# Kernel optimization log

Measured on AMD Instinct MI355X. Metric: run time of the kernel, lower is better.

Reference implementation:

```python
import jax, jax.numpy as jnp
import numpy as np

B, S, D, H, DFF, L, V, LAT = 2, 1800, 128, 8, 512, 6, 16, 1024
DK = D // H


def _pos_encoding():
    # PositionalEncoding buffer, deterministic
    pos = jnp.arange(S, dtype=jnp.float32)[:, None]
    div = jnp.exp(jnp.arange(0, D, 2, dtype=jnp.float32) * (-np.log(10000.0) / D))
    pe = jnp.zeros((S, D), jnp.float32)
    pe = pe.at[:, 0::2].set(jnp.sin(pos * div))
    pe = pe.at[:, 1::2].set(jnp.cos(pos * div))
    return pe  # [S, D]


def _layernorm(x, g, b, eps=1e-5):
    mu = jnp.mean(x, axis=-1, keepdims=True)
    var = jnp.mean((x - mu) ** 2, axis=-1, keepdims=True)
    return (x - mu) / jnp.sqrt(var + eps) * g + b


def _mha(xq, xkv, wq, bq, wk, bk, wv, bv, wo, bo, mask):
    Bq, Sq, _ = xq.shape
    Sk = xkv.shape[1]
    Q = (xq @ wq + bq).reshape(Bq, Sq, H, DK)
    K = (xkv @ wk + bk).reshape(Bq, Sk, H, DK)
    Vv = (xkv @ wv + bv).reshape(Bq, Sk, H, DK)
    scores = jnp.einsum('bqhd,bkhd->bhqk', Q, K) / np.sqrt(DK)
    if mask is not None:
        # faithful to source: masked_fill(mask==0, -1e9) keeps only j>i
        scores = jnp.where(mask, scores, -1e9)
    attn = jax.nn.softmax(scores, axis=-1)
    out = jnp.einsum('bhqk,bkhd->bqhd', attn, Vv).reshape(Bq, Sq, D)
    return out @ wo + bo


def setup_inputs():
    key = jax.random.key(0)
    ks = iter(jax.random.split(key, 40))

    def w(shape, fan_in):
        return (jax.random.normal(next(ks), shape, jnp.float32) / np.sqrt(fan_in))

    inp = {
        'latent': jax.random.normal(next(ks), (B, LAT), jnp.float32),
        'lp_w1': w((LAT, 2 * D), LAT), 'lp_b1': jnp.zeros((2 * D,), jnp.float32),
        'lp_w2': w((2 * D, D * S), 2 * D), 'lp_b2': jnp.zeros((D * S,), jnp.float32),
        'out_w': w((D, V), D), 'out_b': jnp.zeros((V,), jnp.float32),
    }
    for pfx in ('sa', 'ca'):
        for nm in ('q', 'k', 'v', 'o'):
            inp[f'{pfx}_w{nm}'] = w((L, D, D), D)
            inp[f'{pfx}_b{nm}'] = jnp.zeros((L, D), jnp.float32)
    inp['ff_w1'] = w((L, D, DFF), D)
    inp['ff_b1'] = jnp.zeros((L, DFF), jnp.float32)
    inp['ff_w2'] = w((L, DFF, D), DFF)
    inp['ff_b2'] = jnp.zeros((L, D), jnp.float32)
    for i in (1, 2, 3):
        inp[f'ln{i}_g'] = jnp.ones((L, D), jnp.float32)
        inp[f'ln{i}_b'] = jnp.zeros((L, D), jnp.float32)
    return inp


def reference(latent, lp_w1, lp_b1, lp_w2, lp_b2,
              sa_wq, sa_bq, sa_wk, sa_bk, sa_wv, sa_bv, sa_wo, sa_bo,
              ca_wq, ca_bq, ca_wk, ca_bk, ca_wv, ca_bv, ca_wo, ca_bo,
              ff_w1, ff_b1, ff_w2, ff_b2,
              ln1_g, ln1_b, ln2_g, ln2_b, ln3_g, ln3_b,
              out_w, out_b):
    # latent projection -> [B, S, D]
    h = jax.nn.relu(latent @ lp_w1 + lp_b1)
    dec = (h @ lp_w2 + lp_b2).reshape(B, S, D)
    dec = dec + _pos_encoding()[None, :, :]
    # source bug reproduced: only strictly-upper-triangle positions attend
    tgt_mask = jnp.triu(jnp.ones((S, S), bool), 1)
    enc = dec
    x = dec
    for i in range(L):
        a = _mha(x, x, sa_wq[i], sa_bq[i], sa_wk[i], sa_bk[i],
                 sa_wv[i], sa_bv[i], sa_wo[i], sa_bo[i], tgt_mask)
        x = _layernorm(x + a, ln1_g[i], ln1_b[i])
        c = _mha(x, enc, ca_wq[i], ca_bq[i], ca_wk[i], ca_bk[i],
                 ca_wv[i], ca_bv[i], ca_wo[i], ca_bo[i], None)
        x = _layernorm(x + c, ln2_g[i], ln2_b[i])
        f = jax.nn.relu(x @ ff_w1[i] + ff_b1[i]) @ ff_w2[i] + ff_b2[i]
        x = _layernorm(x + f, ln3_g[i], ln3_b[i])
    return x @ out_w + out_b  # [B, S, V]
```

## Files before the change

kernel.cpp:

```cpp
#include <hip/hip_runtime.h>
#include <hip/hip_bf16.h>
#include <math.h>

#define Bn   2
#define Sn   1800
#define Dn   128
#define Hn   8
#define DKn  16
#define DFFn 512
#define Ln   6
#define Vn   16
#define LATn 1024
#define BSn  3600
#define SDn  230400
#define NQT  57
#define VTJ  1824
#define MPAD 3712

typedef __attribute__((ext_vector_type(8))) short short8;
typedef __attribute__((ext_vector_type(16))) float f32x16;
typedef unsigned int u32;
typedef unsigned short u16;

#define ROWMAP(r, hi) (((r) & 3) + 8 * ((r) >> 2) + 4 * (hi))
#define GPERM(sl) (((sl) & 3) + (((sl) & 4) << 1) + (((sl) & 8) >> 1) + ((sl) & 16))

__device__ inline u32 cvtpk_bf16(float a, float b) {
    u32 r;
    asm("v_cvt_pk_bf16_f32 %0, %1, %2" : "=v"(r) : "v"(a), "v"(b));
    return r;
}

__device__ inline u16 f2bf(float f) {
    union { float f; u32 u; } x; x.f = f;
    u32 r = (x.u + 0x7FFFu + ((x.u >> 16) & 1u)) >> 16;
    return (u16)r;
}

__device__ inline float bf2f(u16 v) {
    union { u32 u; float f; } x; x.u = ((u32)v) << 16;
    return x.f;
}

__global__ __launch_bounds__(256) void wconv8_kernel(
    const float* __restrict__ s0, const float* __restrict__ s1,
    const float* __restrict__ s2, const float* __restrict__ s3,
    const float* __restrict__ s4, const float* __restrict__ s5,
    const float* __restrict__ s6, const float* __restrict__ s7,
    u16* __restrict__ d0, u16* __restrict__ d1, u16* __restrict__ d2,
    u16* __restrict__ d3, u16* __restrict__ d4, u16* __restrict__ d5,
    u16* __restrict__ d6, u16* __restrict__ d7)
{
    const int z = blockIdx.z;
    const float* src = (z == 0) ? s0 : (z == 1) ? s1 : (z == 2) ? s2 : (z == 3) ? s3
                     : (z == 4) ? s4 : (z == 5) ? s5 : (z == 6) ? s6 : s7;
    u16* dst = (z == 0) ? d0 : (z == 1) ? d1 : (z == 2) ? d2 : (z == 3) ? d3
             : (z == 4) ? d4 : (z == 5) ? d5 : (z == 6) ? d6 : d7;
    const int id = blockIdx.x * 256 + threadIdx.x;
    const int l = id >> 14, rem = id & 16383;
    const int n = rem >> 7, k = rem & 127;
    dst[id] = f2bf(src[l * 16384 + k * 128 + n]);
}

__global__ __launch_bounds__(256) void wconvg_kernel(
    const float* __restrict__ src, u16* __restrict__ dst, int logK, int logN)
{
    const int id = blockIdx.x * 256 + threadIdx.x;
    const int kn = 1 << (logK + logN);
    const int l = id >> (logK + logN);
    const int rem = id & (kn - 1);
    const int n = rem >> logK, k = rem & ((1 << logK) - 1);
    dst[id] = f2bf(src[(size_t)l * kn + (k << logN) + n]);
}

__global__ __launch_bounds__(256) void zvt_kernel(u16* __restrict__ Vt)
{
    const int id = blockIdx.x * 256 + threadIdx.x;
    const int row = id >> 5, pos = id & 31;
    Vt[(size_t)row * VTJ + 1792 + pos] = 0;
}

__global__ __launch_bounds__(256) void lat_h_kernel(
    const float* __restrict__ latent, const float* __restrict__ w1,
    const float* __restrict__ b1, float* __restrict__ h)
{
    __shared__ float ls[LATn];
    const int b = blockIdx.x;
    const int t = threadIdx.x;
    for (int k = t; k < LATn; k += 256) ls[k] = latent[b * LATn + k];
    __syncthreads();
    float acc = 0.f;
    #pragma unroll 8
    for (int k = 0; k < LATn; ++k) acc = fmaf(ls[k], w1[(size_t)k * 256 + t], acc);
    h[b * 256 + t] = fmaxf(acc + b1[t], 0.f);
}

__global__ __launch_bounds__(256) void dec_kernel(
    const float* __restrict__ h, const float* __restrict__ w2,
    const float* __restrict__ b2, float* __restrict__ x,
    u16* __restrict__ xb, u16* __restrict__ encb)
{
    __shared__ float hs[512];
    const int t = threadIdx.x;
    hs[t] = h[t];
    hs[256 + t] = h[256 + t];
    __syncthreads();
    const int j = blockIdx.x * 256 + t;
    float a0 = 0.f, a1 = 0.f;
    #pragma unroll 8
    for (int k = 0; k < 256; ++k) {
        float w = w2[(size_t)k * SDn + j];
        a0 = fmaf(hs[k], w, a0);
        a1 = fmaf(hs[256 + k], w, a1);
    }
    const int s = j >> 7, d = j & 127;
    const int i2 = d >> 1;
    const float freq = __expf(-(float)(2 * i2) * (9.210340371976184f / 128.f));
    const float ang = (float)s * freq;
    const float pe = (d & 1) ? cosf(ang) : sinf(ang);
    const float bias = b2[j] + pe;
    const float v0 = a0 + bias;
    const float v1 = a1 + bias;
    x[j] = v0;
    x[SDn + j] = v1;
    xb[j] = f2bf(v0);    xb[SDn + j] = f2bf(v1);
    encb[j] = f2bf(v0);  encb[SDn + j] = f2bf(v1);
}

__global__ __launch_bounds__(256) void mm_qkv_kernel(
    const u16* __restrict__ Aq, const u16* __restrict__ Akv,
    const u16* __restrict__ Wq, const u16* __restrict__ Wk, const u16* __restrict__ Wv,
    const float* __restrict__ bq, const float* __restrict__ bk, const float* __restrict__ bv,
    u16* __restrict__ Qb, u16* __restrict__ Kb, u16* __restrict__ Vt)
{
    const int z = blockIdx.z;
    const u16* A = (z == 0) ? Aq : Akv;
    const u16* W = (z == 0) ? Wq : (z == 1) ? Wk : Wv;
    const float* Bi = (z == 0) ? bq : (z == 1) ? bk : bv;

    const int w = threadIdx.x >> 6;
    const int lane = threadIdx.x & 63;
    const int ql = lane & 31, hi = lane >> 5;
    const int m0 = blockIdx.x * 64 + (w & 1) * 32;
    const int nh = (w >> 1) * 64;

    f32x16 acc0 = (f32x16)0.0f, acc1 = (f32x16)0.0f;
    const size_t arow = (size_t)(m0 + ql) * 128;

    #pragma unroll
    for (int kk = 0; kk < 8; ++kk) {
        const short8 a = *(const short8*)(A + arow + kk * 16 + 8 * hi);
        const short8 b0 = *(const short8*)(W + (size_t)(nh + ql) * 128 + kk * 16 + 8 * hi);
        const short8 b1 = *(const short8*)(W + (size_t)(nh + 32 + ql) * 128 + kk * 16 + 8 * hi);
        acc0 = __builtin_amdgcn_mfma_f32_32x32x16_bf16(a, b0, acc0, 0, 0, 0);
        acc1 = __builtin_amdgcn_mfma_f32_32x32x16_bf16(a, b1, acc1, 0, 0, 0);
    }

    #pragma unroll
    for (int j = 0; j < 2; ++j) {
        const int n = nh + j * 32 + ql;
        const float bv_ = Bi[n];
        const int h = n >> 4, d = n & 15;
        #pragma unroll
        for (int r = 0; r < 16; ++r) {
            const int m = m0 + ROWMAP(r, hi);
            if (m >= BSn) continue;
            float v = (j ? acc1[r] : acc0[r]) + bv_;
            const int bq_ = (m >= Sn) ? 1 : 0;
            const int s = m - bq_ * Sn;
            const int bh = bq_ * 8 + h;
            if (z == 0) {
                Qb[((size_t)bh * Sn + s) * 16 + d] = f2bf(v * 0.25f);
            } else if (z == 1) {
                Kb[((size_t)bh * Sn + s) * 16 + d] = f2bf(v);
            } else {
                const int jt = s >> 5, sl = s & 31;
                Vt[((size_t)bh * 16 + d) * VTJ + jt * 32 + GPERM(sl)] = f2bf(v);
            }
        }
    }
}

__device__ inline void ln_stats(const float* ls, float* mus, float* invs, int t)
{
    const int row = t >> 3, q = t & 7;
    float s1 = 0.f, s2 = 0.f;
    const float* lr = &ls[row * 132 + q * 16];
    #pragma unroll
    for (int c = 0; c < 16; c += 4) {
        const float4 v = *(const float4*)&lr[c];
        s1 += v.x + v.y + v.z + v.w;
        s2 += v.x * v.x + v.y * v.y + v.z * v.z + v.w * v.w;
    }
    s1 += __shfl_xor(s1, 1); s2 += __shfl_xor(s2, 1);
    s1 += __shfl_xor(s1, 2); s2 += __shfl_xor(s2, 2);
    s1 += __shfl_xor(s1, 4); s2 += __shfl_xor(s2, 4);
    const float mu = s1 * (1.f / 128.f);
    const float var = s2 * (1.f / 128.f) - mu * mu;
    if (q == 0) { mus[row] = mu; invs[row] = rsqrtf(var + 1e-5f); }
}

__global__ __launch_bounds__(256) void fuse_oln_qkv_kernel(
    const u16* __restrict__ A, const u16* __restrict__ Wo,
    const float* __restrict__ bo,
    const float* __restrict__ g, const float* __restrict__ bb,
    float* __restrict__ X, const u16* __restrict__ Enc,
    const u16* __restrict__ Wq, const u16* __restrict__ Wk, const u16* __restrict__ Wv,
    const float* __restrict__ bq, const float* __restrict__ bk, const float* __restrict__ bv,
    u16* __restrict__ Qb, u16* __restrict__ Kb, u16* __restrict__ Vt)
{
    __shared__ float ls[32 * 132];
    __shared__ float mus[32], invs[32];
    __shared__ alignas(16) u16 ybuf[32][136];

    const int t = threadIdx.x;
    const int w = t >> 6, lane = t & 63;
    const int ql = lane & 31, hi = lane >> 5;
    const int m0 = blockIdx.x * 32;

    {
        f32x16 acc = (f32x16)0.0f;
        const size_t arow = (size_t)(m0 + ql) * 128;
        const int nh = w * 32;
        #pragma unroll
        for (int kk = 0; kk < 8; ++kk) {
            const short8 a = *(const short8*)(A + arow + kk * 16 + 8 * hi);
            const short8 b0 = *(const short8*)(Wo + (size_t)(nh + ql) * 128 + kk * 16 + 8 * hi);
            acc = __builtin_amdgcn_mfma_f32_32x32x16_bf16(a, b0, acc, 0, 0, 0);
        }
        const int n = nh + ql;
        const float bv_ = bo[n];
        #pragma unroll
        for (int r = 0; r < 16; ++r) {
            const int row = ROWMAP(r, hi);
            const int gm = m0 + row;
            float v = acc[r] + bv_;
            if (gm < BSn) v += X[(size_t)gm * 128 + n];
            ls[row * 132 + n] = v;
        }
    }
    __syncthreads();
    ln_stats(ls, mus, invs, t);
    __syncthreads();
    #pragma unroll
    for (int it = 0; it < 4; ++it) {
        const int idx = it * 256 + t;
        const int row = idx >> 5, cg = (idx & 31) * 4;
        const int gm = m0 + row;
        const float4 v = *(const float4*)&ls[row * 132 + cg];
        const float mu = mus[row], inv = invs[row];
        const float4 gv = *(const float4*)&g[cg];
        const float4 bv2 = *(const float4*)&bb[cg];
        float4 y;
        y.x = (v.x - mu) * inv * gv.x + bv2.x;
        y.y = (v.y - mu) * inv * gv.y + bv2.y;
        y.z = (v.z - mu) * inv * gv.z + bv2.z;
        y.w = (v.w - mu) * inv * gv.w + bv2.w;
        if (gm < BSn) *(float4*)&X[(size_t)gm * 128 + cg] = y;
        uint2 u;
        u.x = cvtpk_bf16(y.x, y.y);
        u.y = cvtpk_bf16(y.z, y.w);
        *(uint2*)&ybuf[row][cg] = u;
    }
    __syncthreads();

    #pragma unroll
    for (int z = 0; z < 3; ++z) {
        const u16* W = (z == 0) ? Wq : (z == 1) ? Wk : Wv;
        const float* Bi = (z == 0) ? bq : (z == 1) ? bk : bv;
        f32x16 acc = (f32x16)0.0f;
        const int nh = w * 32;
        #pragma unroll
        for (int kk = 0; kk < 8; ++kk) {
            short8 a;
            if (z == 0) a = *(const short8*)&ybuf[ql][kk * 16 + 8 * hi];
            else        a = *(const short8*)(Enc + (size_t)(m0 + ql) * 128 + kk * 16 + 8 * hi);
            const short8 b0 = *(const short8*)(W + (size_t)(nh + ql) * 128 + kk * 16 + 8 * hi);
            acc = __builtin_amdgcn_mfma_f32_32x32x16_bf16(a, b0, acc, 0, 0, 0);
        }
        const int n = nh + ql;
        const float bv_ = Bi[n];
        const int h = n >> 4, d = n & 15;
        #pragma unroll
        for (int r = 0; r < 16; ++r) {
            const int m = m0 + ROWMAP(r, hi);
            if (m >= BSn) continue;
            float v = acc[r] + bv_;
            const int bq_ = (m >= Sn) ? 1 : 0;
            const int s = m - bq_ * Sn;
            const int bh = bq_ * 8 + h;
            if (z == 0)      Qb[((size_t)bh * Sn + s) * 16 + d] = f2bf(v * 0.25f);
            else if (z == 1) Kb[((size_t)bh * Sn + s) * 16 + d] = f2bf(v);
            else             Vt[((size_t)bh * 16 + d) * VTJ + (s >> 5) * 32 + GPERM(s & 31)] = f2bf(v);
        }
    }
}

template <int WITH_QKV>
__global__ __launch_bounds__(256) void fuse_ffn_kernel(
    const u16* __restrict__ A, const u16* __restrict__ Wo,
    const float* __restrict__ bo,
    const float* __restrict__ g2, const float* __restrict__ b2ln,
    const u16* __restrict__ W1, const float* __restrict__ b1,
    const u16* __restrict__ W2, const float* __restrict__ b2f,
    const float* __restrict__ g3, const float* __restrict__ b3ln,
    float* __restrict__ X,
    const u16* __restrict__ Wq, const u16* __restrict__ Wk, const u16* __restrict__ Wv,
    const float* __restrict__ bq, const float* __restrict__ bk, const float* __restrict__ bv,
    u16* __restrict__ Qb, u16* __restrict__ Kb, u16* __restrict__ Vt)
{
    __shared__ float ls[32 * 132];
    __shared__ float mus[32], invs[32];
    __shared__ alignas(16) u16 ybuf[32][136];
    __shared__ alignas(16) u16 hbuf[32][536];

    const int t = threadIdx.x;
    const int w = t >> 6, lane = t & 63;
    const int ql = lane & 31, hi = lane >> 5;
    const int m0 = blockIdx.x * 32;

    {
        f32x16 acc = (f32x16)0.0f;
        const size_t arow = (size_t)(m0 + ql) * 128;
        const int nh = w * 32;
        #pragma unroll
        for (int kk = 0; kk < 8; ++kk) {
            const short8 a = *(const short8*)(A + arow + kk * 16 + 8 * hi);
            const short8 b0 = *(const short8*)(Wo + (size_t)(nh + ql) * 128 + kk * 16 + 8 * hi);
            acc = __builtin_amdgcn_mfma_f32_32x32x16_bf16(a, b0, acc, 0, 0, 0);
        }
        const int n = nh + ql;
        const float bv_ = bo[n];
        #pragma unroll
        for (int r = 0; r < 16; ++r) {
            const int row = ROWMAP(r, hi);
            const int gm = m0 + row;
            float v = acc[r] + bv_;
            if (gm < BSn) v += X[(size_t)gm * 128 + n];
            ls[row * 132 + n] = v;
        }
    }
    __syncthreads();
    ln_stats(ls, mus, invs, t);
    __syncthreads();
    #pragma unroll
    for (int it = 0; it < 4; ++it) {
        const int idx = it * 256 + t;
        const int row = idx >> 5, cg = (idx & 31) * 4;
        const float4 v = *(const float4*)&ls[row * 132 + cg];
        const float mu = mus[row], inv = invs[row];
        const float4 gv = *(const float4*)&g2[cg];
        const float4 bv2 = *(const float4*)&b2ln[cg];
        float4 y;
        y.x = (v.x - mu) * inv * gv.x + bv2.x;
        y.y = (v.y - mu) * inv * gv.y + bv2.y;
        y.z = (v.z - mu) * inv * gv.z + bv2.z;
        y.w = (v.w - mu) * inv * gv.w + bv2.w;
        *(float4*)&ls[row * 132 + cg] = y;
        uint2 u;
        u.x = cvtpk_bf16(y.x, y.y);
        u.y = cvtpk_bf16(y.z, y.w);
        *(uint2*)&ybuf[row][cg] = u;
    }
    __syncthreads();

    #pragma unroll
    for (int nt = 0; nt < 4; ++nt) {
        const int n0 = w * 128 + nt * 32;
        f32x16 acc = (f32x16)0.0f;
        #pragma unroll
        for (int kk = 0; kk < 8; ++kk) {
            const short8 a = *(const short8*)&ybuf[ql][kk * 16 + 8 * hi];
            const short8 b0 = *(const short8*)(W1 + (size_t)(n0 + ql) * 128 + kk * 16 + 8 * hi);
            acc = __builtin_amdgcn_mfma_f32_32x32x16_bf16(a, b0, acc, 0, 0, 0);
        }
        const int n = n0 + ql;
        const float bv_ = b1[n];
        #pragma unroll
        for (int r = 0; r < 16; ++r) {
            const int row = ROWMAP(r, hi);
            hbuf[row][n] = f2bf(fmaxf(acc[r] + bv_, 0.f));
        }
    }
    __syncthreads();

    {
        f32x16 acc = (f32x16)0.0f;
        const int nh = w * 32;
        #pragma unroll
        for (int kk = 0; kk < 32; ++kk) {
            const short8 a = *(const short8*)&hbuf[ql][kk * 16 + 8 * hi];
            const short8 b0 = *(const short8*)(W2 + (size_t)(nh + ql) * 512 + kk * 16 + 8 * hi);
            acc = __builtin_amdgcn_mfma_f32_32x32x16_bf16(a, b0, acc, 0, 0, 0);
        }
        const int n = nh + ql;
        const float bv_ = b2f[n];
        #pragma unroll
        for (int r = 0; r < 16; ++r) {
            const int row = ROWMAP(r, hi);
            ls[row * 132 + n] = acc[r] + bv_ + ls[row * 132 + n];
        }
    }
    __syncthreads();
    ln_stats(ls, mus, invs, t);
    __syncthreads();
    #pragma unroll
    for (int it = 0; it < 4; ++it) {
        const int idx = it * 256 + t;
        const int row = idx >> 5, cg = (idx & 31) * 4;
        const int gm = m0 + row;
        const float4 v = *(const float4*)&ls[row * 132 + cg];
        const float mu = mus[row], inv = invs[row];
        const float4 gv = *(const float4*)&g3[cg];
        const float4 bv2 = *(const float4*)&b3ln[cg];
        float4 y;
        y.x = (v.x - mu) * inv * gv.x + bv2.x;
        y.y = (v.y - mu) * inv * gv.y + bv2.y;
        y.z = (v.z - mu) * inv * gv.z + bv2.z;
        y.w = (v.w - mu) * inv * gv.w + bv2.w;
        if (gm < BSn) *(float4*)&X[(size_t)gm * 128 + cg] = y;
        uint2 u;
        u.x = cvtpk_bf16(y.x, y.y);
        u.y = cvtpk_bf16(y.z, y.w);
        *(uint2*)&ybuf[row][cg] = u;
    }

    if (WITH_QKV) {
        __syncthreads();
        #pragma unroll
        for (int z = 0; z < 3; ++z) {
            const u16* W = (z == 0) ? Wq : (z == 1) ? Wk : Wv;
            const float* Bi = (z == 0) ? bq : (z == 1) ? bk : bv;
            f32x16 acc = (f32x16)0.0f;
            const int nh = w * 32;
            #pragma unroll
            for (int kk = 0; kk < 8; ++kk) {
                const short8 a = *(const short8*)&ybuf[ql][kk * 16 + 8 * hi];
                const short8 b0 = *(const short8*)(W + (size_t)(nh + ql) * 128 + kk * 16 + 8 * hi);
                acc = __builtin_amdgcn_mfma_f32_32x32x16_bf16(a, b0, acc, 0, 0, 0);
            }
            const int n = nh + ql;
            const float bv_ = Bi[n];
            const int h = n >> 4, d = n & 15;
            #pragma unroll
            for (int r = 0; r < 16; ++r) {
                const int m = m0 + ROWMAP(r, hi);
                if (m >= BSn) continue;
                float v = acc[r] + bv_;
                const int bq_ = (m >= Sn) ? 1 : 0;
                const int s = m - bq_ * Sn;
                const int bh = bq_ * 8 + h;
                if (z == 0)      Qb[((size_t)bh * Sn + s) * 16 + d] = f2bf(v * 0.25f);
                else if (z == 1) Kb[((size_t)bh * Sn + s) * 16 + d] = f2bf(v);
                else             Vt[((size_t)bh * 16 + d) * VTJ + (s >> 5) * 32 + GPERM(s & 31)] = f2bf(v);
            }
        }
    }
}

template <int MASK>
__global__ __launch_bounds__(256) void flash_mfma(
    const u16* __restrict__ Qb, const u16* __restrict__ Kb,
    const u16* __restrict__ Vt, u16* __restrict__ Ob)
{
    __shared__ float mrg[4][64][10];

    const int wid = threadIdx.x >> 6;
    const int lane = threadIdx.x & 63;
    const int bh = blockIdx.y;
    const int b = bh >> 3, h = bh & 7;

    if (MASK && blockIdx.x == NQT) {
        const int d = threadIdx.x & 15, part = threadIdx.x >> 4;
        const u16* row = Vt + ((size_t)bh * 16 + d) * VTJ;
        float s = 0.f;
        for (int j = part; j < VTJ; j += 16) s += bf2f(row[j]);
        ((float*)mrg)[part * 16 + d] = s;
        __syncthreads();
        if (threadIdx.x < 16) {
            float tot = 0.f;
            #pragma unroll
            for (int p = 0; p < 16; ++p) tot += ((float*)mrg)[p * 16 + threadIdx.x];
            Ob[((size_t)(b * Sn + (Sn - 1))) * 128 + h * 16 + threadIdx.x] =
                f2bf(tot * (1.f / (float)Sn));
        }
        return;
    }

    const int ql = lane & 31, hi = lane >> 5;
    const int qt = blockIdx.x;
    const int qrow = qt * 32 + ql;
    const int qr = (qrow < Sn) ? qrow : (Sn - 1);
    const short8 qf = *(const short8*)(Qb + ((size_t)bh * Sn + qr) * 16 + 8 * hi);
    const u16* kbase = Kb + (size_t)bh * Sn * 16;
    const u16* vbase = Vt + ((size_t)bh * 16 + (ql & 15)) * VTJ;

    f32x16 acc = (f32x16)0.0f;
    float m = -INFINITY, lsum = 0.f;

    int jt = (MASK ? qt : 0) + wid;
    short8 kf = (short8)0, va = (short8)0, vb2 = (short8)0;
    if (jt < NQT) {
        int krow = jt * 32 + ql; if (krow >= Sn) krow = Sn - 1;
        kf  = *(const short8*)(kbase + (size_t)krow * 16 + 8 * hi);
        va  = *(const short8*)(vbase + jt * 32 + 8 * hi);
        vb2 = *(const short8*)(vbase + jt * 32 + 16 + 8 * hi);
    }

    for (; jt < NQT; jt += 4) {
        short8 kn = kf, van = va, vbn = vb2;
        if (jt + 4 < NQT) {
            int nrow = (jt + 4) * 32 + ql; if (nrow >= Sn) nrow = Sn - 1;
            kn  = *(const short8*)(kbase + (size_t)nrow * 16 + 8 * hi);
            van = *(const short8*)(vbase + (jt + 4) * 32 + 8 * hi);
            vbn = *(const short8*)(vbase + (jt + 4) * 32 + 16 + 8 * hi);
        }

        const f32x16 sc = __builtin_amdgcn_mfma_f32_32x32x16_bf16(kf, qf, (f32x16)0.0f, 0, 0, 0);

        float sv[16];
        #pragma unroll
        for (int r = 0; r < 16; ++r) sv[r] = sc[r];

        if (MASK && jt == qt) {
            #pragma unroll
            for (int r = 0; r < 16; ++r)
                if (!(ROWMAP(r, hi) > ql)) sv[r] = -1e9f;
        }
        if (jt == NQT - 1) {
            #pragma unroll
            for (int r = 0; r < 16; ++r)
                if (1792 + ROWMAP(r, hi) >= Sn) sv[r] = -1e30f;
        }

        float tmax = sv[0];
        #pragma unroll
        for (int r = 1; r < 16; ++r) tmax = fmaxf(tmax, sv[r]);
        tmax = fmaxf(tmax, __shfl_xor(tmax, 32));
        const float mnew = fmaxf(m, tmax);
        const float corr = __expf(m - mnew);
        m = mnew;
        lsum *= corr;
        #pragma unroll
        for (int r = 0; r < 16; ++r) acc[r] *= corr;

        float p[16];
        float ps = 0.f;
        #pragma unroll
        for (int r = 0; r < 16; ++r) { p[r] = __expf(sv[r] - mnew); ps += p[r]; }
        lsum += ps;

        union { u32 u[4]; short8 s; } B0c, B1c;
        B0c.u[0] = cvtpk_bf16(p[0],  p[1]);  B0c.u[1] = cvtpk_bf16(p[2],  p[3]);
        B0c.u[2] = cvtpk_bf16(p[4],  p[5]);  B0c.u[3] = cvtpk_bf16(p[6],  p[7]);
        B1c.u[0] = cvtpk_bf16(p[8],  p[9]);  B1c.u[1] = cvtpk_bf16(p[10], p[11]);
        B1c.u[2] = cvtpk_bf16(p[12], p[13]); B1c.u[3] = cvtpk_bf16(p[14], p[15]);

        acc = __builtin_amdgcn_mfma_f32_32x32x16_bf16(va,  B0c.s, acc, 0, 0, 0);
        acc = __builtin_amdgcn_mfma_f32_32x32x16_bf16(vb2, B1c.s, acc, 0, 0, 0);

        kf = kn; va = van; vb2 = vbn;
    }

    mrg[wid][lane][0] = m;
    mrg[wid][lane][1] = lsum;
    #pragma unroll
    for (int r = 0; r < 8; ++r) mrg[wid][lane][2 + r] = acc[r];
    __syncthreads();

    if (wid == 0) {
        float mstar = mrg[0][lane][0];
        #pragma unroll
        for (int w2 = 1; w2 < 4; ++w2) mstar = fmaxf(mstar, mrg[w2][lane][0]);
        float lt = 0.f;
        float accf[8] = {};
        #pragma unroll
        for (int w2 = 0; w2 < 4; ++w2) {
            const float sc2 = __expf(mrg[w2][lane][0] - mstar);
            lt += mrg[w2][lane][1] * sc2;
            #pragma unroll
            for (int r = 0; r < 8; ++r) accf[r] = fmaf(mrg[w2][lane][2 + r], sc2, accf[r]);
        }
        const float ltot = lt + __shfl_xor(lt, 32);
        const float inv = 1.f / ltot;
        if (qrow < Sn && !(MASK && qrow == Sn - 1)) {
            u16* op = Ob + ((size_t)(b * Sn + qrow)) * 128 + h * 16;
            uint2 u0, u1;
            u0.x = cvtpk_bf16(accf[0] * inv, accf[1] * inv);
            u0.y = cvtpk_bf16(accf[2] * inv, accf[3] * inv);
            u1.x = cvtpk_bf16(accf[4] * inv, accf[5] * inv);
            u1.y = cvtpk_bf16(accf[6] * inv, accf[7] * inv);
            *(uint2*)(op + 4 * hi) = u0;
            *(uint2*)(op + 8 + 4 * hi) = u1;
        }
    }
}

__global__ __launch_bounds__(256) void out_kernel(
    const float* __restrict__ X, const float* __restrict__ W,
    const float* __restrict__ bb, float* __restrict__ out)
{
    const int t = threadIdx.x;
    const int n = t & 15;
    const int r = blockIdx.x * 16 + (t >> 4);
    if (r >= BSn) return;
    float acc = 0.f;
    #pragma unroll 8
    for (int k = 0; k < 128; ++k)
        acc = fmaf(X[(size_t)r * 128 + k], W[k * 16 + n], acc);
    out[(size_t)r * 16 + n] = acc + bb[n];
}

extern "C" void kernel_launch(void* const* d_in, const int* in_sizes, int n_in,
                              void* d_out, int out_size, void* d_ws, size_t ws_size,
                              hipStream_t stream)
{
    const float* latent = (const float*)d_in[0];
    const float* lp_w1  = (const float*)d_in[1];
    const float* lp_b1  = (const float*)d_in[2];
    const float* lp_w2  = (const float*)d_in[3];
    const float* lp_b2  = (const float*)d_in[4];
    const float* out_w  = (const float*)d_in[5];
    const float* out_b  = (const float*)d_in[6];
    const float* sa_wq = (const float*)d_in[7];  const float* sa_bq = (const float*)d_in[8];
    const float* sa_wk = (const float*)d_in[9];  const float* sa_bk = (const float*)d_in[10];
    const float* sa_wv = (const float*)d_in[11]; const float* sa_bv = (const float*)d_in[12];
    const float* sa_wo = (const float*)d_in[13]; const float* sa_bo = (const float*)d_in[14];
    const float* ca_wq = (const float*)d_in[15]; const float* ca_bq = (const float*)d_in[16];
    const float* ca_wk = (const float*)d_in[17]; const float* ca_bk = (const float*)d_in[18];
    const float* ca_wv = (const float*)d_in[19]; const float* ca_bv = (const float*)d_in[20];
    const float* ca_wo = (const float*)d_in[21]; const float* ca_bo = (const float*)d_in[22];
    const float* ff_w1 = (const float*)d_in[23]; const float* ff_b1 = (const float*)d_in[24];
    const float* ff_w2 = (const float*)d_in[25]; const float* ff_b2 = (const float*)d_in[26];
    const float* ln1g = (const float*)d_in[27]; const float* ln1b = (const float*)d_in[28];
    const float* ln2g = (const float*)d_in[29]; const float* ln2b = (const float*)d_in[30];
    const float* ln3g = (const float*)d_in[31]; const float* ln3b = (const float*)d_in[32];

    float* ws = (float*)d_ws;
    float* x    = ws;
    float* hlat = ws + 460800;
    u16* xb   = (u16*)(ws + 461312);
    u16* encb = (u16*)(ws + 698880);
    u16* ob   = (u16*)(ws + 936448);
    u16* Qb   = (u16*)(ws + 2124288);
    u16* Kb   = (u16*)(ws + 2354688);
    u16* Vt   = (u16*)(ws + 2585088);
    u16* wt_saq = (u16*)(ws + 2818560);
    u16* wt_sak = wt_saq + 6 * 16384;
    u16* wt_sav = wt_sak + 6 * 16384;
    u16* wt_sao = wt_sav + 6 * 16384;
    u16* wt_caq = wt_sao + 6 * 16384;
    u16* wt_cak = wt_caq + 6 * 16384;
    u16* wt_cav = wt_cak + 6 * 16384;
    u16* wt_cao = wt_cav + 6 * 16384;
    u16* wt1  = (u16*)(ws + 3211776);
    u16* wt2  = (u16*)(ws + 3408384);

    wconv8_kernel<<<dim3(384, 1, 8), dim3(256), 0, stream>>>(
        sa_wq, sa_wk, sa_wv, sa_wo, ca_wq, ca_wk, ca_wv, ca_wo,
        wt_saq, wt_sak, wt_sav, wt_sao, wt_caq, wt_cak, wt_cav, wt_cao);
    wconvg_kernel<<<dim3(1536), dim3(256), 0, stream>>>(ff_w1, wt1, 7, 9);
    wconvg_kernel<<<dim3(1536), dim3(256), 0, stream>>>(ff_w2, wt2, 9, 7);
    zvt_kernel<<<dim3(32), dim3(256), 0, stream>>>(Vt);

    lat_h_kernel<<<dim3(2), dim3(256), 0, stream>>>(latent, lp_w1, lp_b1, hlat);
    dec_kernel<<<dim3(900), dim3(256), 0, stream>>>(hlat, lp_w2, lp_b2, x, xb, encb);

    const dim3 thr(256);
    const dim3 gFm(NQT + 1, 16), gFc(NQT, 16), gFuse(113);

    mm_qkv_kernel<<<dim3(57, 1, 3), thr, 0, stream>>>(
        xb, xb, wt_saq, wt_sak, wt_sav, sa_bq, sa_bk, sa_bv, Qb, Kb, Vt);

    for (int i = 0; i < Ln; ++i) {
        const size_t wOff = (size_t)i * 16384;
        const size_t bOff = (size_t)i * 128;
        const size_t fOff = (size_t)i * 65536;
        const size_t f1b  = (size_t)i * 512;
        const size_t wNxt = (size_t)(i + 1) * 16384;
        const size_t bNxt = (size_t)(i + 1) * 128;

        flash_mfma<1><<<gFm, thr, 0, stream>>>(Qb, Kb, Vt, ob);

        fuse_oln_qkv_kernel<<<gFuse, thr, 0, stream>>>(
            ob, wt_sao + wOff, sa_bo + bOff, ln1g + bOff, ln1b + bOff, x, encb,
            wt_caq + wOff, wt_cak + wOff, wt_cav + wOff,
            ca_bq + bOff, ca_bk + bOff, ca_bv + bOff, Qb, Kb, Vt);

        flash_mfma<0><<<gFc, thr, 0, stream>>>(Qb, Kb, Vt, ob);

        if (i < Ln - 1) {
            fuse_ffn_kernel<1><<<gFuse, thr, 0, stream>>>(
                ob, wt_cao + wOff, ca_bo + bOff, ln2g + bOff, ln2b + bOff,
                wt1 + fOff, ff_b1 + f1b, wt2 + fOff, ff_b2 + bOff,
                ln3g + bOff, ln3b + bOff, x,
                wt_saq + wNxt, wt_sak + wNxt, wt_sav + wNxt,
                sa_bq + bNxt, sa_bk + bNxt, sa_bv + bNxt, Qb, Kb, Vt);
        } else {
            fuse_ffn_kernel<0><<<gFuse, thr, 0, stream>>>(
                ob, wt_cao + wOff, ca_bo + bOff, ln2g + bOff, ln2b + bOff,
                wt1 + fOff, ff_b1 + f1b, wt2 + fOff, ff_b2 + bOff,
                ln3g + bOff, ln3b + bOff, x,
                wt_saq, wt_sak, wt_sav, sa_bq, sa_bk, sa_bv, Qb, Kb, Vt);
        }
    }

    out_kernel<<<dim3(225), dim3(256), 0, stream>>>(x, out_w, out_b, (float*)d_out);
}
```

Measured before the change: 616.2 us.

## Merge weight-prep kernels, use exp2 softmax with lazy rescale and MFMA priority

Merges the four weight-conversion and Vt-padding launches into a single kernel to cut launch overhead. It folds log2(e) into the Q scale so the attention softmax can use exp2f instead of __expf. The online-softmax rescale is skipped when no lane's running max changes, and the row max uses a shallower reduction tree. MFMA issue is wrapped in s_setprio to favour matrix work across waves. The risk is a wave-divergent branch plus slightly different rounding from the exp2 path.

```diff
diff --git a/kernel.cpp b/kernel.cpp
--- a/kernel.cpp
+++ b/kernel.cpp
@@ -17,6 +17,8 @@
 #define VTJ  1824
 #define MPAD 3712
 
+#define QSCALE 0.3606737602222409f
+
 typedef __attribute__((ext_vector_type(8))) short short8;
 typedef __attribute__((ext_vector_type(16))) float f32x16;
 typedef unsigned int u32;
@@ -42,42 +44,52 @@
     return x.f;
 }
 
-__global__ __launch_bounds__(256) void wconv8_kernel(
+__device__ inline float xhalf_max(float t) {
+    return fmaxf(t, __shfl_xor(t, 32));
+}
+__device__ inline float xhalf_sum(float t) {
+    return t + __shfl_xor(t, 32);
+}
+
+__global__ __launch_bounds__(256) void wprep_kernel(
     const float* __restrict__ s0, const float* __restrict__ s1,
     const float* __restrict__ s2, const float* __restrict__ s3,
     const float* __restrict__ s4, const float* __restrict__ s5,
     const float* __restrict__ s6, const float* __restrict__ s7,
     u16* __restrict__ d0, u16* __restrict__ d1, u16* __restrict__ d2,
     u16* __restrict__ d3, u16* __restrict__ d4, u16* __restrict__ d5,
-    u16* __restrict__ d6, u16* __restrict__ d7)
-{
-    const int z = blockIdx.z;
-    const float* src = (z == 0) ? s0 : (z == 1) ? s1 : (z == 2) ? s2 : (z == 3) ? s3
-                     : (z == 4) ? s4 : (z == 5) ? s5 : (z == 6) ? s6 : s7;
-    u16* dst = (z == 0) ? d0 : (z == 1) ? d1 : (z == 2) ? d2 : (z == 3) ? d3
-             : (z == 4) ? d4 : (z == 5) ? d5 : (z == 6) ? d6 : d7;
+    u16* __restrict__ d6, u16* __restrict__ d7,
+    const float* __restrict__ f1s, u16* __restrict__ f1d,
+    const float* __restrict__ f2s, u16* __restrict__ f2d,
+    u16* __restrict__ Vt)
+{
     const int id = blockIdx.x * 256 + threadIdx.x;
-    const int l = id >> 14, rem = id & 16383;
-    const int n = rem >> 7, k = rem & 127;
-    dst[id] = f2bf(src[l * 16384 + k * 128 + n]);
-}
-
-__global__ __launch_bounds__(256) void wconvg_kernel(
-    const float* __restrict__ src, u16* __restrict__ dst, int logK, int logN)
-{
-    const int id = blockIdx.x * 256 + threadIdx.x;
-    const int kn = 1 << (logK + logN);
-    const int l = id >> (logK + logN);
-    const int rem = id & (kn - 1);
-    const int n = rem >> logK, k = rem & ((1 << logK) - 1);
-    dst[id] = f2bf(src[(size_t)l * kn + (k << logN) + n]);
-}
-
-__global__ __launch_bounds__(256) void zvt_kernel(u16* __restrict__ Vt)
-{
-    const int id = blockIdx.x * 256 + threadIdx.x;
-    const int row = id >> 5, pos = id & 31;
-    Vt[(size_t)row * VTJ + 1792 + pos] = 0;
+    if (id < 786432) {
+        const int z = id / 98304, rem = id % 98304;
+        const float* src = (z == 0) ? s0 : (z == 1) ? s1 : (z == 2) ? s2 : (z == 3) ? s3
+                         : (z == 4) ? s4 : (z == 5) ? s5 : (z == 6) ? s6 : s7;
+        u16* dst = (z == 0) ? d0 : (z == 1) ? d1 : (z == 2) ? d2 : (z == 3) ? d3
+                 : (z == 4) ? d4 : (z == 5) ? d5 : (z == 6) ? d6 : d7;
+        const int l = rem >> 14, r2 = rem & 16383;
+        const int n = r2 >> 7, k = r2 & 127;
+        dst[rem] = f2bf(src[l * 16384 + k * 128 + n]);
+    } else if (id < 786432 + 393216) {
+        const int rem = id - 786432;
+        const int l = rem >> 16, r2 = rem & 65535;
+        const int n = r2 >> 7, k = r2 & 127;
+        f1d[rem] = f2bf(f1s[(size_t)l * 65536 + k * 512 + n]);
+    } else if (id < 786432 + 786432) {
+        const int rem = id - 786432 - 393216;
+        const int l = rem >> 16, r2 = rem & 65535;
+        const int n = r2 >> 9, k = r2 & 511;
+        f2d[rem] = f2bf(f2s[(size_t)l * 65536 + k * 128 + n]);
+    } else {
+        const int rem = id - 1572864;
+        if (rem < 8192) {
+            const int row = rem >> 5, pos = rem & 31;
+            Vt[(size_t)row * VTJ + 1792 + pos] = 0;
+        }
+    }
 }
 
 __global__ __launch_bounds__(256) void lat_h_kernel(
@@ -170,7 +182,7 @@
             const int s = m - bq_ * Sn;
             const int bh = bq_ * 8 + h;
             if (z == 0) {
-                Qb[((size_t)bh * Sn + s) * 16 + d] = f2bf(v * 0.25f);
+                Qb[((size_t)bh * Sn + s) * 16 + d] = f2bf(v * QSCALE);
             } else if (z == 1) {
                 Kb[((size_t)bh * Sn + s) * 16 + d] = f2bf(v);
             } else {
@@ -289,7 +301,7 @@
             const int bq_ = (m >= Sn) ? 1 : 0;
             const int s = m - bq_ * Sn;
             const int bh = bq_ * 8 + h;
-            if (z == 0)      Qb[((size_t)bh * Sn + s) * 16 + d] = f2bf(v * 0.25f);
+            if (z == 0)      Qb[((size_t)bh * Sn + s) * 16 + d] = f2bf(v * QSCALE);
             else if (z == 1) Kb[((size_t)bh * Sn + s) * 16 + d] = f2bf(v);
             else             Vt[((size_t)bh * 16 + d) * VTJ + (s >> 5) * 32 + GPERM(s & 31)] = f2bf(v);
         }
@@ -450,7 +462,7 @@
                 const int bq_ = (m >= Sn) ? 1 : 0;
                 const int s = m - bq_ * Sn;
                 const int bh = bq_ * 8 + h;
-                if (z == 0)      Qb[((size_t)bh * Sn + s) * 16 + d] = f2bf(v * 0.25f);
+                if (z == 0)      Qb[((size_t)bh * Sn + s) * 16 + d] = f2bf(v * QSCALE);
                 else if (z == 1) Kb[((size_t)bh * Sn + s) * 16 + d] = f2bf(v);
                 else             Vt[((size_t)bh * 16 + d) * VTJ + (s >> 5) * 32 + GPERM(s & 31)] = f2bf(v);
             }
@@ -516,7 +528,9 @@
             vbn = *(const short8*)(vbase + (jt + 4) * 32 + 16 + 8 * hi);
         }
 
+        __builtin_amdgcn_s_setprio(1);
         const f32x16 sc = __builtin_amdgcn_mfma_f32_32x32x16_bf16(kf, qf, (f32x16)0.0f, 0, 0, 0);
+        __builtin_amdgcn_s_setprio(0);
 
         float sv[16];
         #pragma unroll
@@ -533,21 +547,28 @@
                 if (1792 + ROWMAP(r, hi) >= Sn) sv[r] = -1e30f;
         }
 
-        float tmax = sv[0];
-        #pragma unroll
-        for (int r = 1; r < 16; ++r) tmax = fmaxf(tmax, sv[r]);
-        tmax = fmaxf(tmax, __shfl_xor(tmax, 32));
-        const float mnew = fmaxf(m, tmax);
-        const float corr = __expf(m - mnew);
-        m = mnew;
-        lsum *= corr;
-        #pragma unroll
-        for (int r = 0; r < 16; ++r) acc[r] *= corr;
+        const float a0 = fmaxf(fmaxf(sv[0], sv[1]), sv[2]);
+        const float a1 = fmaxf(fmaxf(sv[3], sv[4]), sv[5]);
+        const float a2 = fmaxf(fmaxf(sv[6], sv[7]), sv[8]);
+        const float a3 = fmaxf(fmaxf(sv[9], sv[10]), sv[11]);
+        const float a4 = fmaxf(fmaxf(sv[12], sv[13]), sv[14]);
+        const float b0m = fmaxf(fmaxf(a0, a1), a2);
+        const float b1m = fmaxf(fmaxf(a3, a4), sv[15]);
+        const float tmax = xhalf_max(fmaxf(b0m, b1m));
+
+        if (!__all(tmax <= m)) {
+            const float mnew = fmaxf(m, tmax);
+            const float corr = exp2f(m - mnew);
+            m = mnew;
+            lsum *= corr;
+            #pragma unroll
+            for (int r = 0; r < 16; ++r) acc[r] *= corr;
+        }
 
         float p[16];
         float ps = 0.f;
         #pragma unroll
-        for (int r = 0; r < 16; ++r) { p[r] = __expf(sv[r] - mnew); ps += p[r]; }
+        for (int r = 0; r < 16; ++r) { p[r] = exp2f(sv[r] - m); ps += p[r]; }
         lsum += ps;
 
         union { u32 u[4]; short8 s; } B0c, B1c;
@@ -556,8 +577,10 @@
         B1c.u[0] = cvtpk_bf16(p[8],  p[9]);  B1c.u[1] = cvtpk_bf16(p[10], p[11]);
         B1c.u[2] = cvtpk_bf16(p[12], p[13]); B1c.u[3] = cvtpk_bf16(p[14], p[15]);
 
+        __builtin_amdgcn_s_setprio(1);
         acc = __builtin_amdgcn_mfma_f32_32x32x16_bf16(va,  B0c.s, acc, 0, 0, 0);
         acc = __builtin_amdgcn_mfma_f32_32x32x16_bf16(vb2, B1c.s, acc, 0, 0, 0);
+        __builtin_amdgcn_s_setprio(0);
 
         kf = kn; va = van; vb2 = vbn;
     }
@@ -576,12 +599,12 @@
         float accf[8] = {};
         #pragma unroll
         for (int w2 = 0; w2 < 4; ++w2) {
-            const float sc2 = __expf(mrg[w2][lane][0] - mstar);
+            const float sc2 = exp2f(mrg[w2][lane][0] - mstar);
             lt += mrg[w2][lane][1] * sc2;
             #pragma unroll
             for (int r = 0; r < 8; ++r) accf[r] = fmaf(mrg[w2][lane][2 + r], sc2, accf[r]);
         }
-        const float ltot = lt + __shfl_xor(lt, 32);
+        const float ltot = xhalf_sum(lt);
         const float inv = 1.f / ltot;
         if (qrow < Sn && !(MASK && qrow == Sn - 1)) {
             u16* op = Ob + ((size_t)(b * Sn + qrow)) * 128 + h * 16;
@@ -656,12 +679,10 @@
     u16* wt1  = (u16*)(ws + 3211776);
     u16* wt2  = (u16*)(ws + 3408384);
 
-    wconv8_kernel<<<dim3(384, 1, 8), dim3(256), 0, stream>>>(
+    wprep_kernel<<<dim3(6176), dim3(256), 0, stream>>>(
         sa_wq, sa_wk, sa_wv, sa_wo, ca_wq, ca_wk, ca_wv, ca_wo,
-        wt_saq, wt_sak, wt_sav, wt_sao, wt_caq, wt_cak, wt_cav, wt_cao);
-    wconvg_kernel<<<dim3(1536), dim3(256), 0, stream>>>(ff_w1, wt1, 7, 9);
-    wconvg_kernel<<<dim3(1536), dim3(256), 0, stream>>>(ff_w2, wt2, 9, 7);
-    zvt_kernel<<<dim3(32), dim3(256), 0, stream>>>(Vt);
+        wt_saq, wt_sak, wt_sav, wt_sao, wt_caq, wt_cak, wt_cav, wt_cao,
+        ff_w1, wt1, ff_w2, wt2, Vt);
 
     lat_h_kernel<<<dim3(2), dim3(256), 0, stream>>>(latent, lp_w1, lp_b1, hlat);
     dec_kernel<<<dim3(900), dim3(256), 0, stream>>>(hlat, lp_w2, lp_b2, x, xb, encb);
```

New measurement: 664.8 us. 1.08x slower.
